# Performance work log

Measured on AMD Instinct MI355X. Metric: run time of the kernel, lower is better.

## Reference

```python
import jax, jax.numpy as jnp
import numpy as np

B, N, F_DIM, M, K, D = 8, 16384, 6, 128, 16, 768
MLP_DIMS = [F_DIM, 256, 512, 768, D]


def _fps(pts):
    """Deterministic farthest point sampling. pts: [N,4] -> indices [M] (first pick = point 0)."""
    n = pts.shape[0]

    def step(carry, _):
        min_d, last = carry
        d = jnp.sum((pts - pts[last]) ** 2, axis=-1)
        min_d = jnp.minimum(min_d, d)
        nxt = jnp.argmax(min_d).astype(jnp.int32)
        return (min_d, nxt), nxt

    init = (jnp.full((n,), 1e30, dtype=pts.dtype), jnp.int32(0))
    _, idx = jax.lax.scan(step, init, None, length=M - 1)
    return jnp.concatenate([jnp.zeros((1,), jnp.int32), idx])


def setup_inputs() -> dict:
    key = jax.random.key(0)
    ks = jax.random.split(key, 16)
    bidx = jnp.repeat(jnp.arange(B, dtype=jnp.float32), N)[:, None]
    xyzt = jax.random.normal(ks[0], (B * N, 4), jnp.float32)
    coordinates = jnp.concatenate([bidx, xyzt], axis=1)  # [B*N, 5]
    features = jax.random.normal(ks[1], (B * N, F_DIM), jnp.float32)
    inp = {"coordinates": coordinates, "features": features}
    for i in range(4):
        di, do = MLP_DIMS[i], MLP_DIMS[i + 1]
        inp[f"W{i}"] = jax.random.normal(ks[2 + i], (di, do), jnp.float32) * np.float32(1.0 / np.sqrt(di))
        inp[f"b{i}"] = jnp.zeros((do,), jnp.float32)
    for j in range(2):
        inp[f"Wn{j}"] = jax.random.normal(ks[6 + j], (D, D), jnp.float32) * np.float32(1.0 / np.sqrt(D))
        inp[f"bn{j}"] = jnp.zeros((D,), jnp.float32)
    return inp


def _forward(coordinates, features, W0, b0, W1, b1, W2, b2, W3, b3, Wn0, bn0, Wn1, bn1):
    # Equal points per event, sorted batch ids -> plain reshape replaces the per-batch loop.
    pts = coordinates.reshape(B, N, 5)[:, :, 1:5]       # xyz + time  [B,N,4]
    h = features.reshape(B, N, F_DIM)
    # per-point MLP (ReLU after each hidden layer, final Linear has no activation)
    h = jax.nn.relu(h @ W0 + b0)
    h = jax.nn.relu(h @ W1 + b1)
    h = jax.nn.relu(h @ W2 + b2)
    pf = h @ W3 + b3                                    # [B,N,D]
    # FPS centroids (non-differentiable index selection, as in the torch/cpu original)
    fidx = jax.vmap(_fps)(jax.lax.stop_gradient(pts))   # [B,M]
    cent = jnp.take_along_axis(pts, fidx[:, :, None], axis=1)  # [B,M,4]
    # cdist + kNN (smallest distances)
    dist = jnp.sqrt(jnp.sum((cent[:, :, None, :] - pts[:, None, :, :]) ** 2, axis=-1))  # [B,M,N]
    _, knn = jax.lax.top_k(-dist, K)                    # [B,M,K]
    gathered = jax.vmap(lambda p, i: p[i])(pf, knn)     # [B,M,K,D]
    pooled = jnp.max(gathered, axis=2)                  # [B,M,D]
    t = jax.nn.relu(pooled @ Wn0 + bn0)
    tokens = t @ Wn1 + bn1                              # [B,M,D]
    # sort tokens/centroids by centroid time (column 3)
    order = jnp.argsort(cent[:, :, 3], axis=1)
    cent = jnp.take_along_axis(cent, order[:, :, None], axis=1)
    tokens = jnp.take_along_axis(tokens, order[:, :, None], axis=1)
    masks = jnp.ones((B, M), dtype=bool)  # num_points > max_tokens -> all tokens valid
    return tokens, cent, masks


def reference(coordinates, features, W0, b0, W1, b1, W2, b2, W3, b3, Wn0, bn0, Wn1, bn1):
    return _forward(coordinates, features, W0, b0, W1, b1, W2, b2, W3, b3, Wn0, bn0, Wn1, bn1)
```

## Files before the change

### kernel.cpp

```cpp
#include <hip/hip_runtime.h>

#define B_ 8
#define N_ 16384
#define F_ 6
#define M_ 128
#define K_ 16
#define D_ 768

typedef unsigned short u16;
typedef unsigned int u32;
typedef __attribute__((ext_vector_type(8))) short short8;
typedef __attribute__((ext_vector_type(4))) float f32x4;
typedef __attribute__((ext_vector_type(2))) float f32x2;

__device__ __forceinline__ u16 f2bf(float f){
  union { float f; u32 i; } v; v.f = f;
  u32 x = v.i;
  u32 r = x + 0x7FFFu + ((x >> 16) & 1u);
  return (u16)(r >> 16);
}

__global__ __launch_bounds__(256) void conv_wt(const float* __restrict__ W,
                                               u16* __restrict__ WT, int K, int N){
  __shared__ u16 tile[64][65];
  int tiles_n = N >> 6;
  int tk = blockIdx.x / tiles_n, tn = blockIdx.x % tiles_n;
  int k0 = tk << 6, n0 = tn << 6;
  int t = threadIdx.x;
#pragma unroll
  for (int q = 0; q < 16; q++){
    int idx = q * 256 + t;
    int kk = idx >> 6, nn = idx & 63;
    tile[kk][nn] = f2bf(W[(size_t)(k0 + kk) * N + n0 + nn]);
  }
  __syncthreads();
#pragma unroll
  for (int q = 0; q < 16; q++){
    int idx = q * 256 + t;
    int nn = idx >> 6, kk = idx & 63;
    WT[(size_t)(n0 + nn) * K + k0 + kk] = tile[kk][nn];
  }
}

__global__ __launch_bounds__(1024) void fps_kernel(const float* __restrict__ coords,
                                                   float* __restrict__ cent){
#pragma clang fp contract(off)
  __shared__ f32x4 sxy[N_ / 2];
  __shared__ float s_wv[2][16];
  __shared__ int s_wi[2][16];
  int b = blockIdx.x;
  int t = threadIdx.x;
  const float* cb = coords + (size_t)b * N_ * 5;
  f32x2 pz[8], pw[8], md[8];
#pragma unroll
  for (int j = 0; j < 8; j++){
    int p = t + (j << 10);
    size_t i0 = (size_t)(2 * p) * 5, i1 = i0 + 5;
    f32x4 v; v[0] = cb[i0+1]; v[1] = cb[i1+1]; v[2] = cb[i0+2]; v[3] = cb[i1+2];
    sxy[p] = v;
    pz[j] = (f32x2){cb[i0+3], cb[i1+3]};
    pw[j] = (f32x2){cb[i0+4], cb[i1+4]};
    md[j] = (f32x2){1e30f, 1e30f};
  }
  float cx = cb[1], cy = cb[2], cz = cb[3], ct = cb[4];
  if (t == 0){
    float* c0 = cent + (size_t)b * M_ * 4;
    c0[0]=cx; c0[1]=cy; c0[2]=cz; c0[3]=ct;
  }
  __syncthreads();
  for (int step = 1; step < M_; step++){
    f32x2 cx2 = (f32x2){cx, cx}, cy2 = (f32x2){cy, cy};
    f32x2 cz2 = (f32x2){cz, cz}, ct2 = (f32x2){ct, ct};
    float bv = -1.0f; int bi = 1 << 30;
#pragma unroll
    for (int j = 0; j < 8; j++){
      int p = t + (j << 10);
      f32x4 v = sxy[p];
      f32x2 X = (f32x2){v[0], v[1]};
      f32x2 Y = (f32x2){v[2], v[3]};
      f32x2 dX = X - cx2;
      f32x2 dY = Y - cy2;
      f32x2 s = dX*dX + dY*dY;
      f32x2 dZ = pz[j] - cz2;
      s = s + dZ*dZ;
      f32x2 dW = pw[j] - ct2;
      s = s + dW*dW;
      f32x2 m = md[j];
      m[0] = (s[0] < m[0]) ? s[0] : m[0];
      m[1] = (s[1] < m[1]) ? s[1] : m[1];
      md[j] = m;
      int i0 = p << 1;
      if (m[0] > bv){ bv = m[0]; bi = i0; }
      if (m[1] > bv){ bv = m[1]; bi = i0 + 1; }
    }
#pragma unroll
    for (int off = 32; off > 0; off >>= 1){
      float ov = __shfl_down(bv, off);
      int oi = __shfl_down(bi, off);
      if (ov > bv || (ov == bv && oi < bi)){ bv = ov; bi = oi; }
    }
    int par = step & 1;
    if ((t & 63) == 0){ s_wv[par][t >> 6] = bv; s_wi[par][t >> 6] = bi; }
    __syncthreads();
    float fv = s_wv[par][t & 15];
    int fi = s_wi[par][t & 15];
#pragma unroll
    for (int off = 1; off < 16; off <<= 1){
      float ov = __shfl_xor(fv, off);
      int oi = __shfl_xor(fi, off);
      if (ov > fv || (ov == fv && oi < fi)){ fv = ov; fi = oi; }
    }
    fi &= (N_ - 1);
    f32x4 vw = sxy[fi >> 1];
    int odd = fi & 1;
    cx = odd ? vw[1] : vw[0];
    cy = odd ? vw[3] : vw[2];
    cz = cb[(size_t)fi*5+3];
    ct = cb[(size_t)fi*5+4];
    if (t == 0){
      float* cr = cent + ((size_t)b * M_ + step) * 4;
      cr[0]=cx; cr[1]=cy; cr[2]=cz; cr[3]=ct;
    }
  }
}

__global__ __launch_bounds__(128) void rank_scatter(const float* __restrict__ cent_fps,
                                                    float* __restrict__ cent_sorted,
                                                    float* __restrict__ out,
                                                    size_t out_elems){
  int b = blockIdx.x, m = threadIdx.x;
  __shared__ float tt[M_];
  const float* row = cent_fps + ((size_t)b * M_ + m) * 4;
  float x=row[0], y=row[1], z=row[2], w=row[3];
  tt[m] = w;
  __syncthreads();
  int rank = 0;
  for (int j = 0; j < M_; j++){
    float tj = tt[j];
    if (tj < w || (tj == w && j < m)) rank++;
  }
  float* dst = cent_sorted + ((size_t)b * M_ + rank) * 4;
  dst[0]=x; dst[1]=y; dst[2]=z; dst[3]=w;
  size_t co = (size_t)B_ * M_ * D_ + ((size_t)b * M_ + rank) * 4;
  if (co + 3 < out_elems){
    out[co+0]=x; out[co+1]=y; out[co+2]=z; out[co+3]=w;
  }
  size_t mo = (size_t)B_ * M_ * D_ + (size_t)B_ * M_ * 4 + (size_t)b * M_ + m;
  if (mo < out_elems) out[mo] = 1.0f;
}

#define KNT 512
#define KPT 32
__global__ __launch_bounds__(512) void knn_kernel(const float* __restrict__ coords,
                                                  const float* __restrict__ cent,
                                                  int* __restrict__ knn){
#pragma clang fp contract(off)
  int cm = blockIdx.x;
  int b = cm >> 7;
  const float* cb = coords + (size_t)b * N_ * 5;
  int t = threadIdx.x;
  float cx=cent[cm*4+0], cy=cent[cm*4+1], cz=cent[cm*4+2], ct=cent[cm*4+3];
  float dist[KPT];
#pragma unroll
  for (int j = 0; j < KPT; j++){
    size_t i = t + j * KNT;
    float dx=cb[i*5+1]-cx, dy=cb[i*5+2]-cy, dz=cb[i*5+3]-cz, dw=cb[i*5+4]-ct;
    float d = ((dx*dx + dy*dy) + dz*dz) + dw*dw;
    dist[j] = sqrtf(d);
  }
  __shared__ float s_wv[8];
  __shared__ int s_wi[8];
  __shared__ int s_bi;
  for (int r = 0; r < K_; r++){
    float bv = 3e38f; int bi = 1 << 30;
#pragma unroll
    for (int j = 0; j < KPT; j++){
      int i = t + j * KNT;
      float v = dist[j];
      if (v < bv){ bv = v; bi = i; }
    }
#pragma unroll
    for (int off = 32; off > 0; off >>= 1){
      float ov = __shfl_down(bv, off);
      int oi = __shfl_down(bi, off);
      if (ov < bv || (ov == bv && oi < bi)){ bv = ov; bi = oi; }
    }
    if ((t & 63) == 0){ s_wv[t >> 6] = bv; s_wi[t >> 6] = bi; }
    __syncthreads();
    if (t == 0){
      float fv = s_wv[0]; int fi = s_wi[0];
      for (int w = 1; w < 8; w++){
        float wv = s_wv[w]; int wi = s_wi[w];
        if (wv < fv || (wv == fv && wi < fi)){ fv = wv; fi = wi; }
      }
      s_bi = fi;
      knn[(size_t)cm * K_ + r] = fi & (N_ - 1);
    }
    __syncthreads();
    int wi = s_bi;
#pragma unroll
    for (int j = 0; j < KPT; j++){
      if (t + j * KNT == wi) dist[j] = 3e38f;
    }
  }
}

__global__ __launch_bounds__(256) void gather_l0(const float* __restrict__ feat,
                                                 const int* __restrict__ knn,
                                                 const float* __restrict__ W0,
                                                 const float* __restrict__ b0,
                                                 u16* __restrict__ h1,
                                                 int rowBase){
  int lrow = blockIdx.x;
  int grow = rowBase + lrow;
  int b = grow >> 11;
  int t = threadIdx.x;
  __shared__ float sf[F_];
  if (t < F_){
    int idx = knn[grow] & (N_ - 1);
    sf[t] = feat[((size_t)b * N_ + idx) * F_ + t];
  }
  __syncthreads();
  float acc = b0[t];
#pragma unroll
  for (int k = 0; k < F_; k++) acc = fmaf(sf[k], W0[k * 256 + t], acc);
  h1[(size_t)lrow * 256 + t] = f2bf(fmaxf(acc, 0.0f));
}

template<int RELU, int OUTF32>
__global__ __launch_bounds__(256) void gemm_bf16(const u16* __restrict__ A,
                                                 const u16* __restrict__ WT,
                                                 const float* __restrict__ bias,
                                                 void* __restrict__ Cv,
                                                 int Kd, int Nd){
  __shared__ u16 As[128][40];
  __shared__ u16 Bs[128][40];
  const int t = threadIdx.x;
  const int bm = blockIdx.y << 7;
  const int bn = blockIdx.x << 7;
  const int wave = t >> 6;
  const int lane = t & 63;
  const int wm = (wave & 1) << 6;
  const int wn = (wave >> 1) << 6;
  const int lm = lane & 15;
  const int lk = (lane >> 4) << 3;
  f32x4 acc[4][4] = {};
  for (int k0 = 0; k0 < Kd; k0 += 32){
#pragma unroll
    for (int it = 0; it < 2; it++){
      int slot = t + (it << 8);
      int r = slot >> 2;
      int c = (slot & 3) << 3;
      short8 v = *(const short8*)(A + (size_t)(bm + r) * Kd + k0 + c);
      *(short8*)&As[r][c] = v;
      short8 w = *(const short8*)(WT + (size_t)(bn + r) * Kd + k0 + c);
      *(short8*)&Bs[r][c] = w;
    }
    __syncthreads();
    short8 af[4], bfr[4];
#pragma unroll
    for (int mt = 0; mt < 4; mt++) af[mt] = *(const short8*)&As[wm + (mt << 4) + lm][lk];
#pragma unroll
    for (int nt = 0; nt < 4; nt++) bfr[nt] = *(const short8*)&Bs[wn + (nt << 4) + lm][lk];
#pragma unroll
    for (int mt = 0; mt < 4; mt++)
#pragma unroll
      for (int nt = 0; nt < 4; nt++)
        acc[mt][nt] = __builtin_amdgcn_mfma_f32_16x16x32_bf16(af[mt], bfr[nt], acc[mt][nt], 0, 0, 0);
    __syncthreads();
  }
#pragma unroll
  for (int nt = 0; nt < 4; nt++){
    int n = bn + wn + (nt << 4) + lm;
    float bia = bias[n];
#pragma unroll
    for (int mt = 0; mt < 4; mt++){
#pragma unroll
      for (int r2 = 0; r2 < 4; r2++){
        int m = bm + wm + (mt << 4) + ((lane >> 4) << 2) + r2;
        float v = acc[mt][nt][r2] + bia;
        if (RELU) v = fmaxf(v, 0.0f);
        if (OUTF32) ((float*)Cv)[(size_t)m * Nd + n] = v;
        else        ((u16*)Cv)[(size_t)m * Nd + n] = f2bf(v);
      }
    }
  }
}

template<int RELU, int OUTF32>
__global__ __launch_bounds__(256) void gemm64(const u16* __restrict__ A,
                                              const u16* __restrict__ WT,
                                              const float* __restrict__ bias,
                                              void* __restrict__ Cv,
                                              int Kd, int Nd){
  __shared__ u16 As[64][40];
  __shared__ u16 Bs[64][40];
  const int t = threadIdx.x;
  const int bm = blockIdx.y << 6;
  const int bn = blockIdx.x << 6;
  const int wave = t >> 6;
  const int lane = t & 63;
  const int wm = (wave & 1) << 5;
  const int wn = (wave >> 1) << 5;
  const int lm = lane & 15;
  const int lk = (lane >> 4) << 3;
  f32x4 acc[2][2] = {};
  for (int k0 = 0; k0 < Kd; k0 += 32){
    {
      int r = t >> 2;
      int c = (t & 3) << 3;
      short8 v = *(const short8*)(A + (size_t)(bm + r) * Kd + k0 + c);
      *(short8*)&As[r][c] = v;
      short8 w = *(const short8*)(WT + (size_t)(bn + r) * Kd + k0 + c);
      *(short8*)&Bs[r][c] = w;
    }
    __syncthreads();
    short8 af[2], bfr[2];
#pragma unroll
    for (int mt = 0; mt < 2; mt++) af[mt] = *(const short8*)&As[wm + (mt << 4) + lm][lk];
#pragma unroll
    for (int nt = 0; nt < 2; nt++) bfr[nt] = *(const short8*)&Bs[wn + (nt << 4) + lm][lk];
#pragma unroll
    for (int mt = 0; mt < 2; mt++)
#pragma unroll
      for (int nt = 0; nt < 2; nt++)
        acc[mt][nt] = __builtin_amdgcn_mfma_f32_16x16x32_bf16(af[mt], bfr[nt], acc[mt][nt], 0, 0, 0);
    __syncthreads();
  }
#pragma unroll
  for (int nt = 0; nt < 2; nt++){
    int n = bn + wn + (nt << 4) + lm;
    float bia = bias[n];
#pragma unroll
    for (int mt = 0; mt < 2; mt++){
#pragma unroll
      for (int r2 = 0; r2 < 4; r2++){
        int m = bm + wm + (mt << 4) + ((lane >> 4) << 2) + r2;
        float v = acc[mt][nt][r2] + bia;
        if (RELU) v = fmaxf(v, 0.0f);
        if (OUTF32) ((float*)Cv)[(size_t)m * Nd + n] = v;
        else        ((u16*)Cv)[(size_t)m * Nd + n] = f2bf(v);
      }
    }
  }
}

__global__ __launch_bounds__(256) void gemm_pool(const u16* __restrict__ A,
                                                 const u16* __restrict__ WT,
                                                 const float* __restrict__ bias,
                                                 u16* __restrict__ pooled,
                                                 int Kd, int Nd, int groupBase){
  __shared__ u16 As[128][40];
  __shared__ u16 Bs[128][40];
  const int t = threadIdx.x;
  const int bm = blockIdx.y << 7;
  const int bn = blockIdx.x << 7;
  const int wave = t >> 6;
  const int lane = t & 63;
  const int wm = (wave & 1) << 6;
  const int wn = (wave >> 1) << 6;
  const int lm = lane & 15;
  const int lk = (lane >> 4) << 3;
  f32x4 acc[4][4] = {};
  for (int k0 = 0; k0 < Kd; k0 += 32){
#pragma unroll
    for (int it = 0; it < 2; it++){
      int slot = t + (it << 8);
      int r = slot >> 2;
      int c = (slot & 3) << 3;
      short8 v = *(const short8*)(A + (size_t)(bm + r) * Kd + k0 + c);
      *(short8*)&As[r][c] = v;
      short8 w = *(const short8*)(WT + (size_t)(bn + r) * Kd + k0 + c);
      *(short8*)&Bs[r][c] = w;
    }
    __syncthreads();
    short8 af[4], bfr[4];
#pragma unroll
    for (int mt = 0; mt < 4; mt++) af[mt] = *(const short8*)&As[wm + (mt << 4) + lm][lk];
#pragma unroll
    for (int nt = 0; nt < 4; nt++) bfr[nt] = *(const short8*)&Bs[wn + (nt << 4) + lm][lk];
#pragma unroll
    for (int mt = 0; mt < 4; mt++)
#pragma unroll
      for (int nt = 0; nt < 4; nt++)
        acc[mt][nt] = __builtin_amdgcn_mfma_f32_16x16x32_bf16(af[mt], bfr[nt], acc[mt][nt], 0, 0, 0);
    __syncthreads();
  }
#pragma unroll
  for (int nt = 0; nt < 4; nt++){
    int n = bn + wn + (nt << 4) + lm;
    float bia = bias[n];
#pragma unroll
    for (int mt = 0; mt < 4; mt++){
      f32x4 a = acc[mt][nt];
      float v = fmaxf(fmaxf(a[0], a[1]), fmaxf(a[2], a[3]));
      v = fmaxf(v, __shfl_xor(v, 16));
      v = fmaxf(v, __shfl_xor(v, 32));
      if ((lane >> 4) == 0){
        int g = groupBase + (bm >> 4) + (wm >> 4) + mt;
        pooled[(size_t)g * Nd + n] = f2bf(v + bia);
      }
    }
  }
}

__global__ __launch_bounds__(256) void fill_diag(float* __restrict__ out, size_t out_elems){
  size_t i = (size_t)blockIdx.x * 256 + threadIdx.x;
  if (i >= out_elems) return;
  size_t maskStart = (size_t)B_ * M_ * D_ + (size_t)B_ * M_ * 4;
  out[i] = (i >= maskStart) ? 1.0f : 0.0f;
}

extern "C" void kernel_launch(void* const* d_in, const int* in_sizes, int n_in,
                              void* d_out, int out_size, void* d_ws, size_t ws_size,
                              hipStream_t stream){
  (void)in_sizes; (void)n_in;
  const float* coords   = (const float*)d_in[0];
  const float* features = (const float*)d_in[1];
  const float* W0 = (const float*)d_in[2];  const float* b0 = (const float*)d_in[3];
  const float* W1 = (const float*)d_in[4];  const float* b1 = (const float*)d_in[5];
  const float* W2 = (const float*)d_in[6];  const float* b2 = (const float*)d_in[7];
  const float* W3 = (const float*)d_in[8];  const float* b3 = (const float*)d_in[9];
  const float* Wn0 = (const float*)d_in[10]; const float* bn0 = (const float*)d_in[11];
  const float* Wn1 = (const float*)d_in[12]; const float* bn1 = (const float*)d_in[13];
  float* out = (float*)d_out;
  const size_t out_elems = (size_t)out_size;

  char* ws = (char*)d_ws;
  const size_t o_cent = 0;
  const size_t o_cntS = 16384;
  const size_t o_knn  = 32768;
  const size_t o_Wb   = 131072;
  const size_t o_pool = 4718592;
  const size_t o_t1   = 6291456;
  const size_t o_chunk= 7864320;
  const int ROWS = B_ * M_ * K_;

  int R = 16384;
  while (R > 128 && o_chunk + (size_t)R * 2560 > ws_size) R >>= 1;
  if (d_ws == nullptr || o_chunk + (size_t)R * 2560 > ws_size){
    fill_diag<<<(int)((out_elems + 255) / 256), 256, 0, stream>>>(out, out_elems);
    return;
  }

  float* cent_fps    = (float*)(ws + o_cent);
  float* cent_sorted = (float*)(ws + o_cntS);
  int*   knn         = (int*)(ws + o_knn);
  u16* Wb   = (u16*)(ws + o_Wb);
  u16* W1t  = Wb;               u16* W2t  = Wb + 131072;
  u16* W3t  = Wb + 524288;      u16* Wn0t = Wb + 1114112;
  u16* Wn1t = Wb + 1703936;
  u16* pooled = (u16*)(ws + o_pool);
  u16* t1     = (u16*)(ws + o_t1);
  u16* regA   = (u16*)(ws + o_chunk);
  u16* regB   = (u16*)(ws + o_chunk + (size_t)R * 1536);

  conv_wt<<< 32, 256, 0, stream>>>(W1,  W1t,  256, 512);
  conv_wt<<< 96, 256, 0, stream>>>(W2,  W2t,  512, 768);
  conv_wt<<<144, 256, 0, stream>>>(W3,  W3t,  768, 768);
  conv_wt<<<144, 256, 0, stream>>>(Wn0, Wn0t, 768, 768);
  conv_wt<<<144, 256, 0, stream>>>(Wn1, Wn1t, 768, 768);

  fps_kernel<<<B_, 1024, 0, stream>>>(coords, cent_fps);
  rank_scatter<<<B_, 128, 0, stream>>>(cent_fps, cent_sorted, out, out_elems);
  knn_kernel<<<B_ * M_, KNT, 0, stream>>>(coords, cent_sorted, knn);

  for (int rowBase = 0; rowBase < ROWS; rowBase += R){
    gather_l0<<<R, 256, 0, stream>>>(features, knn, W0, b0, regA, rowBase);
    gemm_bf16<1,0><<<dim3(4, R / 128), 256, 0, stream>>>(regA, W1t, b1, regB, 256, 512);
    gemm_bf16<1,0><<<dim3(6, R / 128), 256, 0, stream>>>(regB, W2t, b2, regA, 512, 768);
    gemm_pool<<<dim3(6, R / 128), 256, 0, stream>>>(regA, W3t, b3, pooled, 768, 768, rowBase >> 4);
  }

  gemm64<1,0><<<dim3(12, (B_ * M_) / 64), 256, 0, stream>>>(pooled, Wn0t, bn0, t1, 768, 768);
  gemm64<0,1><<<dim3(12, (B_ * M_) / 64), 256, 0, stream>>>(t1, Wn1t, bn1, out, 768, 768);
}
```

Before: 597.6 us.

## Keep FPS points fully in registers with 512 threads; batch gather_l0 rows per block

The FPS kernel drops the shared-memory xy array and instead holds all four coordinates of 32 points per thread in registers, using 512 threads per block, so the per-step cross-wave reduction covers 8 waves instead of 16. The selected centroid is re-read from global memory instead of shared memory. Separately, gather_l0 now handles 32 rows per block and stages W0/b0 in shared memory, which cuts the block count and the redundant weight loads. The risks are higher register pressure and a global-memory load latency sitting on the serial FPS critical path at every step.

```diff
diff --git a/kernel.cpp b/kernel.cpp
--- a/kernel.cpp
+++ b/kernel.cpp
@@ -42,24 +42,24 @@
   }
 }
 
-__global__ __launch_bounds__(1024) void fps_kernel(const float* __restrict__ coords,
-                                                   float* __restrict__ cent){
+#define FPW 16
+__global__ __launch_bounds__(512, 2) void fps_kernel(const float* __restrict__ coords,
+                                                     float* __restrict__ cent){
 #pragma clang fp contract(off)
-  __shared__ f32x4 sxy[N_ / 2];
-  __shared__ float s_wv[2][16];
-  __shared__ int s_wi[2][16];
+  __shared__ float s_wv[2][8];
+  __shared__ int s_wi[2][8];
   int b = blockIdx.x;
   int t = threadIdx.x;
   const float* cb = coords + (size_t)b * N_ * 5;
-  f32x2 pz[8], pw[8], md[8];
-#pragma unroll
-  for (int j = 0; j < 8; j++){
-    int p = t + (j << 10);
-    size_t i0 = (size_t)(2 * p) * 5, i1 = i0 + 5;
-    f32x4 v; v[0] = cb[i0+1]; v[1] = cb[i1+1]; v[2] = cb[i0+2]; v[3] = cb[i1+2];
-    sxy[p] = v;
-    pz[j] = (f32x2){cb[i0+3], cb[i1+3]};
-    pw[j] = (f32x2){cb[i0+4], cb[i1+4]};
+  f32x2 px[FPW], py[FPW], pz[FPW], pw[FPW], md[FPW];
+#pragma unroll
+  for (int j = 0; j < FPW; j++){
+    int p = t + (j << 9);
+    size_t i0 = (size_t)(2 * p) * 5;
+    px[j] = (f32x2){cb[i0+1], cb[i0+6]};
+    py[j] = (f32x2){cb[i0+2], cb[i0+7]};
+    pz[j] = (f32x2){cb[i0+3], cb[i0+8]};
+    pw[j] = (f32x2){cb[i0+4], cb[i0+9]};
     md[j] = (f32x2){1e30f, 1e30f};
   }
   float cx = cb[1], cy = cb[2], cz = cb[3], ct = cb[4];
@@ -67,19 +67,14 @@
     float* c0 = cent + (size_t)b * M_ * 4;
     c0[0]=cx; c0[1]=cy; c0[2]=cz; c0[3]=ct;
   }
-  __syncthreads();
   for (int step = 1; step < M_; step++){
     f32x2 cx2 = (f32x2){cx, cx}, cy2 = (f32x2){cy, cy};
     f32x2 cz2 = (f32x2){cz, cz}, ct2 = (f32x2){ct, ct};
     float bv = -1.0f; int bi = 1 << 30;
 #pragma unroll
-    for (int j = 0; j < 8; j++){
-      int p = t + (j << 10);
-      f32x4 v = sxy[p];
-      f32x2 X = (f32x2){v[0], v[1]};
-      f32x2 Y = (f32x2){v[2], v[3]};
-      f32x2 dX = X - cx2;
-      f32x2 dY = Y - cy2;
+    for (int j = 0; j < FPW; j++){
+      f32x2 dX = px[j] - cx2;
+      f32x2 dY = py[j] - cy2;
       f32x2 s = dX*dX + dY*dY;
       f32x2 dZ = pz[j] - cz2;
       s = s + dZ*dZ;
@@ -89,7 +84,7 @@
       m[0] = (s[0] < m[0]) ? s[0] : m[0];
       m[1] = (s[1] < m[1]) ? s[1] : m[1];
       md[j] = m;
-      int i0 = p << 1;
+      int i0 = (t + (j << 9)) << 1;
       if (m[0] > bv){ bv = m[0]; bi = i0; }
       if (m[1] > bv){ bv = m[1]; bi = i0 + 1; }
     }
@@ -102,21 +97,17 @@
     int par = step & 1;
     if ((t & 63) == 0){ s_wv[par][t >> 6] = bv; s_wi[par][t >> 6] = bi; }
     __syncthreads();
-    float fv = s_wv[par][t & 15];
-    int fi = s_wi[par][t & 15];
-#pragma unroll
-    for (int off = 1; off < 16; off <<= 1){
+    float fv = s_wv[par][t & 7];
+    int fi = s_wi[par][t & 7];
+#pragma unroll
+    for (int off = 1; off < 8; off <<= 1){
       float ov = __shfl_xor(fv, off);
       int oi = __shfl_xor(fi, off);
       if (ov > fv || (ov == fv && oi < fi)){ fv = ov; fi = oi; }
     }
     fi &= (N_ - 1);
-    f32x4 vw = sxy[fi >> 1];
-    int odd = fi & 1;
-    cx = odd ? vw[1] : vw[0];
-    cy = odd ? vw[3] : vw[2];
-    cz = cb[(size_t)fi*5+3];
-    ct = cb[(size_t)fi*5+4];
+    size_t wbase = (size_t)fi * 5;
+    cx = cb[wbase+1]; cy = cb[wbase+2]; cz = cb[wbase+3]; ct = cb[wbase+4];
     if (t == 0){
       float* cr = cent + ((size_t)b * M_ + step) * 4;
       cr[0]=cx; cr[1]=cy; cr[2]=cz; cr[3]=ct;
@@ -211,20 +202,29 @@
                                                  const float* __restrict__ b0,
                                                  u16* __restrict__ h1,
                                                  int rowBase){
-  int lrow = blockIdx.x;
-  int grow = rowBase + lrow;
-  int b = grow >> 11;
+  __shared__ float sW[F_][256];
+  __shared__ float sb[256];
+  __shared__ float sfa[32][F_];
   int t = threadIdx.x;
-  __shared__ float sf[F_];
-  if (t < F_){
+#pragma unroll
+  for (int k = 0; k < F_; k++) sW[k][t] = W0[k * 256 + t];
+  sb[t] = b0[t];
+  if (t < 32 * F_){
+    int r = t / F_, k = t % F_;
+    int grow = rowBase + blockIdx.x * 32 + r;
+    int bb = grow >> 11;
     int idx = knn[grow] & (N_ - 1);
-    sf[t] = feat[((size_t)b * N_ + idx) * F_ + t];
+    sfa[r][k] = feat[((size_t)bb * N_ + idx) * F_ + k];
   }
   __syncthreads();
-  float acc = b0[t];
-#pragma unroll
-  for (int k = 0; k < F_; k++) acc = fmaf(sf[k], W0[k * 256 + t], acc);
-  h1[(size_t)lrow * 256 + t] = f2bf(fmaxf(acc, 0.0f));
+#pragma unroll 4
+  for (int r = 0; r < 32; r++){
+    float acc = sb[t];
+#pragma unroll
+    for (int k = 0; k < F_; k++) acc = fmaf(sfa[r][k], sW[k][t], acc);
+    int lrow = blockIdx.x * 32 + r;
+    h1[(size_t)lrow * 256 + t] = f2bf(fmaxf(acc, 0.0f));
+  }
 }
 
 template<int RELU, int OUTF32>
@@ -461,12 +461,12 @@
   conv_wt<<<144, 256, 0, stream>>>(Wn0, Wn0t, 768, 768);
   conv_wt<<<144, 256, 0, stream>>>(Wn1, Wn1t, 768, 768);
 
-  fps_kernel<<<B_, 1024, 0, stream>>>(coords, cent_fps);
+  fps_kernel<<<B_, 512, 0, stream>>>(coords, cent_fps);
   rank_scatter<<<B_, 128, 0, stream>>>(cent_fps, cent_sorted, out, out_elems);
   knn_kernel<<<B_ * M_, KNT, 0, stream>>>(coords, cent_sorted, knn);
 
   for (int rowBase = 0; rowBase < ROWS; rowBase += R){
-    gather_l0<<<R, 256, 0, stream>>>(features, knn, W0, b0, regA, rowBase);
+    gather_l0<<<R / 32, 256, 0, stream>>>(features, knn, W0, b0, regA, rowBase);
     gemm_bf16<1,0><<<dim3(4, R / 128), 256, 0, stream>>>(regA, W1t, b1, regB, 256, 512);
     gemm_bf16<1,0><<<dim3(6, R / 128), 256, 0, stream>>>(regB, W2t, b2, regA, 512, 768);
     gemm_pool<<<dim3(6, R / 128), 256, 0, stream>>>(regA, W3t, b3, pooled, 768, 768, rowBase >> 4);
```

After: 571.3 us. -4.4%, faster.
